# Kernel optimization log

Measured on AMD Instinct MI355X. Metric: run time of the kernel, lower is better.

The kernel has to match this reference:

```python
import jax, jax.numpy as jnp
import numpy as np

EPS = 1e-5
THRESHOLD = 0.2987


def conv3x3(x, w, stride=1):
    # x: [N,C,H,W], w: [O,I,3,3]
    return jax.lax.conv_general_dilated(
        x, w, window_strides=(stride, stride), padding=((1, 1), (1, 1)),
        dimension_numbers=("NCHW", "OIHW", "NCHW"))


def batchnorm_train(x, gamma, beta):
    # training-mode BN: batch statistics over (N,H,W), biased variance
    mean = jnp.mean(x, axis=(0, 2, 3), keepdims=True)
    var = jnp.var(x, axis=(0, 2, 3), keepdims=True)
    xhat = (x - mean) * jax.lax.rsqrt(var + EPS)
    return xhat * gamma[None, :, None, None] + beta[None, :, None, None]


def setup_inputs() -> dict:
    key = jax.random.key(0)
    k = jax.random.split(key, 7)
    N, C, H, W = 64, 128, 64, 64
    x = jax.random.normal(k[0], (N, C, H, W), dtype=jnp.float32)
    w1 = jax.random.normal(k[1], (C, C, 3, 3), dtype=jnp.float32) * (1.0 / np.sqrt(C * 9))
    gamma1 = jnp.ones((C,), dtype=jnp.float32)
    beta1 = jnp.zeros((C,), dtype=jnp.float32)
    w2 = jax.random.normal(k[2], (C, C, 3, 3), dtype=jnp.float32) * (1.0 / np.sqrt(C * 9))
    gamma2 = jnp.ones((C,), dtype=jnp.float32)
    beta2 = jnp.zeros((C,), dtype=jnp.float32)
    return {"x": x, "w1": w1, "gamma1": gamma1, "beta1": beta1,
            "w2": w2, "gamma2": gamma2, "beta2": beta2}


def reference(x, w1, gamma1, beta1, w2, gamma2, beta2):
    shortcut = x  # stride=1, no down_sample
    out = conv3x3(x, w1, stride=1)
    out = batchnorm_train(out, gamma1, beta1)
    out = jax.nn.relu(out)
    # per-(batch,channel) mean over H,W; zero channels whose mean < threshold
    channel_means = jnp.mean(out, axis=(2, 3))               # [N, C]
    mask = (channel_means >= THRESHOLD).astype(out.dtype)     # [N, C]
    out = out * mask[:, :, None, None]
    out = conv3x3(out, w2, stride=1)
    out = batchnorm_train(out, gamma2, beta2)
    out = out + shortcut
    out = jax.nn.relu(out)
    return out
```

## Files before the change

kernel.cpp:

```cpp
#include <hip/hip_runtime.h>

typedef short short8 __attribute__((ext_vector_type(8)));
typedef short short4v __attribute__((ext_vector_type(4)));
typedef float f32x4 __attribute__((ext_vector_type(4)));
typedef unsigned int u32;

#define EPSF 1e-5f
#define THRF 0.2987f

constexpr int N_ = 64, C_ = 128;
constexpr int PLANE = 4096;
constexpr size_t TENSOR = (size_t)N_ * C_ * PLANE;
constexpr int NHW = N_ * PLANE;
constexpr int PUNITS = 66 * 66 * 8;

__device__ __forceinline__ unsigned short f2bf(float f) {
    unsigned u = __float_as_uint(f);
    u += 0x7fffu + ((u >> 16) & 1u);
    return (unsigned short)(u >> 16);
}
__device__ __forceinline__ float bf2f(unsigned short h) {
    return __uint_as_float((unsigned)h << 16);
}
__device__ __forceinline__ void gld16(const unsigned short* g, unsigned short* l) {
    __builtin_amdgcn_global_load_lds(
        (const __attribute__((address_space(1))) u32*)g,
        (__attribute__((address_space(3))) u32*)l, 16, 0, 0);
}

__global__ __launch_bounds__(256) void prep_w_k(const float* __restrict__ w1,
                                                const float* __restrict__ w2,
                                                unsigned short* __restrict__ Wt1,
                                                unsigned short* __restrict__ Wt2) {
    int idx = blockIdx.x * 256 + threadIdx.x;
    const int sel = idx >= 147456;
    const float* src = sel ? w2 : w1;
    unsigned short* dst = sel ? Wt2 : Wt1;
    const int r = idx - sel * 147456;
    const int tap = r >> 14;
    const int rem = r & 16383;
    const int co = rem >> 7, ci = rem & 127;
    const int half = ci >> 6, csh = (ci >> 5) & 1;
    const int s = half * 18 + tap * 2 + csh;
    dst[(size_t)s * 4096 + co * 32 + (ci & 31)] = f2bf(src[(co * 128 + ci) * 9 + tap]);
}

__global__ __launch_bounds__(256) void zero_border_k(unsigned short* __restrict__ io) {
    int idx = blockIdx.x * 256 + threadIdx.x;
    if (idx >= 266240) return;
    const int plane = idx / 2080;
    const int t = idx - plane * 2080;
    int sp;
    if (t < 528) sp = t >> 3;
    else if (t < 1056) sp = 65 * 66 + ((t - 528) >> 3);
    else if (t < 1568) sp = (((t - 1056) >> 3) + 1) * 66;
    else sp = (((t - 1568) >> 3) + 1) * 66 + 65;
    const size_t off = ((size_t)plane * PUNITS + sp * 8 + (t & 7)) * 8;
    *(short8*)&io[off] = (short8){0, 0, 0, 0, 0, 0, 0, 0};
}

__global__ __launch_bounds__(256) void to_nhwc_k(const float* __restrict__ src,
                                                 unsigned short* __restrict__ dst) {
    __shared__ __align__(16) unsigned short tl[64 * 40];
    const int b = blockIdx.x;
    const int c0 = (b & 3) * 32;
    const int h  = (b >> 2) & 63;
    const int n  = b >> 8;
    const int t  = threadIdx.x;
    for (int i = t; i < 512; i += 256) {
        const int cl = i >> 4;
        const int c  = c0 + cl;
        const int w4 = (i & 15) * 4;
        float4 v = *(const float4*)&src[(size_t)(n * 128 + c) * 4096 + h * 64 + w4];
        tl[(w4 + 0) * 40 + cl] = f2bf(v.x);
        tl[(w4 + 1) * 40 + cl] = f2bf(v.y);
        tl[(w4 + 2) * 40 + cl] = f2bf(v.z);
        tl[(w4 + 3) * 40 + cl] = f2bf(v.w);
    }
    __syncthreads();
    const int w = t >> 2, cs = t & 3;
    short8 v = *(const short8*)&tl[w * 40 + cs * 8];
    const int c = c0 + cs * 8;
    const int half = c >> 6, cig = (c >> 3) & 7;
    const int colp = w + 1, rowp = h + 1;
    const size_t off = ((size_t)(half * 64 + n) * PUNITS
                        + (size_t)(rowp * 66 + colp) * 8 + (cig ^ (colp & 7))) * 8;
    *(short8*)&dst[off] = v;
}

template <int STAGE>
__global__ __launch_bounds__(256, 3) void conv_mfma_k(
    const unsigned short* __restrict__ inT, const unsigned short* __restrict__ Wt,
    const float* __restrict__ msA, const float* __restrict__ mhA,
    unsigned short* __restrict__ outB, float* __restrict__ part) {
    __shared__ __align__(16) unsigned short sIn[2112 * 8];
    __shared__ float fS[256], fQ[256];

    const int b  = (blockIdx.x & 7) * 256 + (blockIdx.x >> 3);
    const int h0 = (b & 31) * 2;
    const int n  = b >> 5;
    const int tid  = threadIdx.x;
    const int lane = tid & 63;
    const int wid  = tid >> 6;
    const int co_base = (wid >> 1) * 64;
    const int px_base = (wid & 1) * 64;
    const int lr = lane & 15;
    const int lg = lane >> 4;

    f32x4 acc[4][4];
#pragma unroll
    for (int i = 0; i < 4; ++i)
#pragma unroll
        for (int j = 0; j < 4; ++j) acc[i][j] = (f32x4){0.f, 0.f, 0.f, 0.f};

    const int nc = n * 128;
    const unsigned short* wlane = Wt + (size_t)(co_base + lr) * 32 + lg * 8;

    int ldsQ[4][2][3];
#pragma unroll
    for (int j = 0; j < 4; ++j) {
        const int px = px_base + j * 16 + lr;
        const int r = px >> 6, c = px & 63;
#pragma unroll
        for (int csh = 0; csh < 2; ++csh)
#pragma unroll
            for (int dc = 0; dc < 3; ++dc) {
                const int cig = csh * 4 + lg;
                ldsQ[j][csh][dc] = (r * 66 + c + dc) * 128 + (cig ^ ((c + dc) & 7)) * 16;
            }
    }

    auto stage_in = [&](int half) {
        const unsigned short* src =
            inT + ((size_t)(half * 64 + n) * PUNITS + (size_t)h0 * 66 * 8) * 8;
        if (STAGE == 1) {
            for (int c = wid; c < 33; c += 4)
                gld16(src + (c * 64 + lane) * 8, &sIn[c * 512]);
        } else {
            const int ncb = nc + half * 64;
            for (int i = tid; i < 2112; i += 256) {
                const int sp = i >> 3, ul = i & 7;
                const int rq = sp / 66;
                const int colp = sp - rq * 66;
                const int rp = h0 + rq;
                short8 v = {0, 0, 0, 0, 0, 0, 0, 0};
                if (rp != 0 && rp != 65 && colp != 0 && colp != 65) {
                    v = *(const short8*)&src[i * 8];
                    const int cig = ul ^ (colp & 7);
                    const int cb = ncb + cig * 8;
                    const float4 m0 = *(const float4*)&msA[cb];
                    const float4 m1 = *(const float4*)&msA[cb + 4];
                    const float4 a0 = *(const float4*)&mhA[cb];
                    const float4 a1 = *(const float4*)&mhA[cb + 4];
                    short8 w;
                    w[0] = (short)f2bf(fmaxf(fmaf(bf2f((unsigned short)v[0]), m0.x, a0.x), 0.f));
                    w[1] = (short)f2bf(fmaxf(fmaf(bf2f((unsigned short)v[1]), m0.y, a0.y), 0.f));
                    w[2] = (short)f2bf(fmaxf(fmaf(bf2f((unsigned short)v[2]), m0.z, a0.z), 0.f));
                    w[3] = (short)f2bf(fmaxf(fmaf(bf2f((unsigned short)v[3]), m0.w, a0.w), 0.f));
                    w[4] = (short)f2bf(fmaxf(fmaf(bf2f((unsigned short)v[4]), m1.x, a1.x), 0.f));
                    w[5] = (short)f2bf(fmaxf(fmaf(bf2f((unsigned short)v[5]), m1.y, a1.y), 0.f));
                    w[6] = (short)f2bf(fmaxf(fmaf(bf2f((unsigned short)v[6]), m1.z, a1.z), 0.f));
                    w[7] = (short)f2bf(fmaxf(fmaf(bf2f((unsigned short)v[7]), m1.w, a1.w), 0.f));
                    v = w;
                }
                *(short8*)&sIn[i * 8] = v;
            }
        }
    };

    auto ldw2 = [&](short8* dst, const unsigned short* p) {
#pragma unroll
        for (int i = 0; i < 4; ++i)
            dst[i] = *(const short8*)&p[i * 512];
    };
    auto ldb = [&](short8* bfv, int dr, int dc, int csh) {
#pragma unroll
        for (int j = 0; j < 4; ++j)
            bfv[j] = *(const short8*)((const char*)sIn + ldsQ[j][csh][dc] + dr * 8448);
    };
    auto mm = [&](short8* af, short8* bfv) {
        __builtin_amdgcn_s_setprio(1);
#pragma unroll
        for (int i = 0; i < 4; ++i)
#pragma unroll
            for (int j = 0; j < 4; ++j)
                acc[i][j] = __builtin_amdgcn_mfma_f32_16x16x32_bf16(af[i], bfv[j],
                                                                    acc[i][j], 0, 0, 0);
        __builtin_amdgcn_s_setprio(0);
    };

    short8 afA[4], afB[4], bfv[4];
    const unsigned short* wpA = wlane;
    const unsigned short* wpB = wlane + 4096;

    stage_in(0);
    ldw2(afA, wpA);
    ldw2(afB, wpB);
    __syncthreads();

#pragma unroll
    for (int half = 0; half < 2; ++half) {
#pragma unroll
        for (int it = 0; it < 9; ++it) {
            const int dr = it / 3, dc = it - dr * 3;
            ldb(bfv, dr, dc, 0);
            mm(afA, bfv);
            if (it < 8) { wpA += 8192; ldw2(afA, wpA); }
            ldb(bfv, dr, dc, 1);
            mm(afB, bfv);
            if (it < 8) { wpB += 8192; ldw2(afB, wpB); }
        }
        if (half == 0) {
            wpA += 8192; ldw2(afA, wpA);
            wpB += 8192; ldw2(afB, wpB);
            __syncthreads();
            stage_in(1);
            __syncthreads();
        }
    }

#pragma unroll
    for (int i = 0; i < 4; ++i)
#pragma unroll
        for (int q = 0; q < 4; ++q) {
            float v = acc[i][0][q] + acc[i][1][q] + acc[i][2][q] + acc[i][3][q];
            float w = acc[i][0][q] * acc[i][0][q] + acc[i][1][q] * acc[i][1][q]
                    + acc[i][2][q] * acc[i][2][q] + acc[i][3][q] * acc[i][3][q];
#pragma unroll
            for (int m = 1; m < 16; m <<= 1) {
                v += __shfl_xor(v, m);
                w += __shfl_xor(w, m);
            }
            if (lr == 0) {
                const int colocal = i * 16 + lg * 4 + q;
                fS[wid * 64 + colocal] = v;
                fQ[wid * 64 + colocal] = w;
            }
        }
    __syncthreads();
    if (tid < 128) {
        const int grp = tid >> 6, cl = tid & 63;
        part[(size_t)b * 256 + tid]       = fS[(grp * 2) * 64 + cl] + fS[(grp * 2 + 1) * 64 + cl];
        part[(size_t)b * 256 + 128 + tid] = fQ[(grp * 2) * 64 + cl] + fQ[(grp * 2 + 1) * 64 + cl];
    }

    if (STAGE == 1) {
        const int h = h0 + (px_base >> 6);
        const int rowp = h + 1;
        const size_t plane = (size_t)((co_base >> 6) * 64 + n) * PUNITS * 8;
        const int pg = lg >> 1;
#pragma unroll
        for (int j = 0; j < 4; ++j) {
            const int w = j * 16 + lr;
            const int colp = w + 1;
            const size_t spoff = plane + (size_t)(rowp * 66 + colp) * 8 * 8;
#pragma unroll
            for (int i = 0; i < 4; ++i) {
                u32 p0 = ((u32)f2bf(acc[i][j][1]) << 16) | f2bf(acc[i][j][0]);
                u32 p1 = ((u32)f2bf(acc[i][j][3]) << 16) | f2bf(acc[i][j][2]);
                const u32 q0 = __shfl_xor(p0, 16);
                const u32 q1 = __shfl_xor(p1, 16);
                if ((lg & 1) == 0) {
                    const int cig = (i * 2 + pg) & 7;
                    u32 st4[4] = {p0, p1, q0, q1};
                    *(short8*)&outB[spoff + (size_t)(cig ^ (colp & 7)) * 8] =
                        *(const short8*)st4;
                }
            }
        }
    } else {
        const size_t outN = (size_t)n * 128 * 4096;
#pragma unroll
        for (int i = 0; i < 4; ++i) {
            const int cob = co_base + i * 16 + lg * 4;
#pragma unroll
            for (int q = 0; q < 4; ++q) {
                unsigned short* op = outB + outN + (size_t)(cob + q) * 4096
                                     + h0 * 64 + px_base + lr;
#pragma unroll
                for (int j = 0; j < 4; ++j) op[j * 16] = f2bf(acc[i][j][q]);
            }
        }
    }
}

__global__ __launch_bounds__(256) void bn_finalize_k(const float* __restrict__ part,
                                                     const float* __restrict__ gamma,
                                                     const float* __restrict__ beta,
                                                     float* __restrict__ st) {
    const int c = blockIdx.x;
    float s = 0.f, q = 0.f;
    for (int b = threadIdx.x; b < 2048; b += 256) {
        s += part[(size_t)b * 256 + c];
        q += part[(size_t)b * 256 + 128 + c];
    }
    __shared__ float rs[256], rq[256];
    rs[threadIdx.x] = s; rq[threadIdx.x] = q;
    __syncthreads();
    for (int o = 128; o > 0; o >>= 1) {
        if (threadIdx.x < o) {
            rs[threadIdx.x] += rs[threadIdx.x + o];
            rq[threadIdx.x] += rq[threadIdx.x + o];
        }
        __syncthreads();
    }
    if (threadIdx.x == 0) {
        const float inv  = 1.f / (float)NHW;
        const float mean = rs[0] * inv;
        const float var  = rq[0] * inv - mean * mean;
        const float sc   = gamma[c] * rsqrtf(var + EPSF);
        st[c]       = sc;
        st[C_ + c]  = fmaf(-mean, sc, beta[c]);
    }
}

__global__ __launch_bounds__(256) void maskpart_k(const unsigned short* __restrict__ y1,
                                                  const float* __restrict__ st,
                                                  float* __restrict__ qsum) {
    const int n = blockIdx.x >> 1, half = blockIdx.x & 1;
    const int t = threadIdx.x;
    const int colg = t & 63;
    const int p = t >> 6;
    const int colp = 1 + colg;
    float scv[2][8], shv[2][8], a[2][8];
#pragma unroll
    for (int k = 0; k < 2; ++k)
#pragma unroll
        for (int e = 0; e < 8; ++e) {
            const int c = half * 64 + (2 * p + k) * 8 + e;
            scv[k][e] = st[c];
            shv[k][e] = st[128 + c];
            a[k][e] = 0.f;
        }
    const size_t plane = (size_t)(half * 64 + n) * PUNITS * 8;
    for (int rowp = 1; rowp <= 64; ++rowp) {
        const int sp = rowp * 66 + colp;
#pragma unroll
        for (int k = 0; k < 2; ++k) {
            const int cig = 2 * p + k;
            short8 v = *(const short8*)&y1[plane + ((size_t)sp * 8 + (cig ^ (colp & 7))) * 8];
#pragma unroll
            for (int e = 0; e < 8; ++e)
                a[k][e] += fmaxf(fmaf(bf2f((unsigned short)v[e]), scv[k][e], shv[k][e]), 0.f);
        }
    }
    __shared__ float lds[256][16];
#pragma unroll
    for (int k = 0; k < 2; ++k)
#pragma unroll
        for (int e = 0; e < 8; ++e) lds[t][k * 8 + e] = a[k][e];
    __syncthreads();
    if (t < 64) {
        const int cig = t >> 3, e = t & 7, p2 = cig >> 1, k2 = cig & 1;
        float s = 0.f;
        for (int cg = 0; cg < 64; ++cg) s += lds[p2 * 64 + cg][k2 * 8 + e];
        qsum[(size_t)(n * 2 + half) * 64 + t] = s;
    }
}

__global__ void maskfin_k(const float* __restrict__ qsum, const float* __restrict__ st,
                          float* __restrict__ msA, float* __restrict__ mhA) {
    const int n = blockIdx.x, c = threadIdx.x;
    if (c >= 128) return;
    const int half = c >> 6, cl = c & 63;
    const float s = qsum[(size_t)(n * 2 + half) * 64 + cl];
    const float m = (s * (1.f / 4096.f) >= THRF) ? 1.f : 0.f;
    msA[n * 128 + c] = st[c] * m;
    mhA[n * 128 + c] = st[128 + c] * m;
}

__global__ __launch_bounds__(256) void final_k(const unsigned short* __restrict__ y3,
                                               const float* __restrict__ x,
                                               const float* __restrict__ st,
                                               float* __restrict__ out) {
    const size_t total8 = TENSOR / 8;
    for (size_t g = (size_t)blockIdx.x * 256 + threadIdx.x; g < total8;
         g += (size_t)gridDim.x * 256) {
        const int c = (int)((g >> 9) & (C_ - 1));
        const float sc = st[c], sh = st[C_ + c];
        short8 yv = *(const short8*)&y3[g * 8];
        float4 a0 = ((const float4*)x)[g * 2];
        float4 a1 = ((const float4*)x)[g * 2 + 1];
        float4 o0, o1;
        o0.x = fmaxf(fmaf(bf2f((unsigned short)yv[0]), sc, sh) + a0.x, 0.f);
        o0.y = fmaxf(fmaf(bf2f((unsigned short)yv[1]), sc, sh) + a0.y, 0.f);
        o0.z = fmaxf(fmaf(bf2f((unsigned short)yv[2]), sc, sh) + a0.z, 0.f);
        o0.w = fmaxf(fmaf(bf2f((unsigned short)yv[3]), sc, sh) + a0.w, 0.f);
        o1.x = fmaxf(fmaf(bf2f((unsigned short)yv[4]), sc, sh) + a1.x, 0.f);
        o1.y = fmaxf(fmaf(bf2f((unsigned short)yv[5]), sc, sh) + a1.y, 0.f);
        o1.z = fmaxf(fmaf(bf2f((unsigned short)yv[6]), sc, sh) + a1.z, 0.f);
        o1.w = fmaxf(fmaf(bf2f((unsigned short)yv[7]), sc, sh) + a1.w, 0.f);
        ((float4*)out)[g * 2]     = o0;
        ((float4*)out)[g * 2 + 1] = o1;
    }
}

extern "C" void kernel_launch(void* const* d_in, const int* in_sizes, int n_in,
                              void* d_out, int out_size, void* d_ws, size_t ws_size,
                              hipStream_t stream) {
    const float* x  = (const float*)d_in[0];
    const float* w1 = (const float*)d_in[1];
    const float* g1 = (const float*)d_in[2];
    const float* b1 = (const float*)d_in[3];
    const float* w2 = (const float*)d_in[4];
    const float* g2 = (const float*)d_in[5];
    const float* b2 = (const float*)d_in[6];
    float* out = (float*)d_out;

    unsigned short* y1 = (unsigned short*)d_out;

    char* wsb = (char*)d_ws;
    unsigned short* io  = (unsigned short*)wsb;
    unsigned short* y3b = (unsigned short*)wsb;
    unsigned short* Wt1 = (unsigned short*)(wsb + (size_t)71368704);
    unsigned short* Wt2 = Wt1 + 147456;
    float* part  = (float*)(wsb + (size_t)71368704 + 589824);
    float* st1   = part + 2048 * 256;
    float* st2   = st1 + 256;
    float* qsum  = st2 + 256;
    float* msA   = qsum + 128 * 64;
    float* mhA   = msA + 64 * 128;

    prep_w_k<<<1152, 256, 0, stream>>>(w1, w2, Wt1, Wt2);
    zero_border_k<<<1040, 256, 0, stream>>>(io);
    to_nhwc_k<<<16384, 256, 0, stream>>>(x, io);
    conv_mfma_k<1><<<2048, 256, 0, stream>>>(io, Wt1, nullptr, nullptr, y1, part);
    bn_finalize_k<<<128, 256, 0, stream>>>(part, g1, b1, st1);
    maskpart_k<<<128, 256, 0, stream>>>(y1, st1, qsum);
    maskfin_k<<<64, 128, 0, stream>>>(qsum, st1, msA, mhA);
    conv_mfma_k<2><<<2048, 256, 0, stream>>>(y1, Wt2, msA, mhA, y3b, part);
    bn_finalize_k<<<128, 256, 0, stream>>>(part, g2, b2, st2);
    final_k<<<8192, 256, 0, stream>>>(y3b, x, st2, out);
}
```

Measured before the change: 329.9 us.

## Fuse NCHW-to-bf16 conversion and border padding into first conv staging; merge mask kernels

The first conv now reads fp32 NCHW input directly, converts it to bf16, and writes the swizzled padded tile into LDS with zero halo. This replaces the separate zero_border and to_nhwc passes and the padded intermediate buffer. The mask finalize step is folded into maskpart_k, which removes another launch. The trade-off is that conv1 staging now does strided scalar fp32 loads (8 channels per plane stride) instead of async 16-byte global-to-LDS loads, and each halo row is re-read and re-converted by neighbouring blocks.

```diff
diff --git a/kernel.cpp b/kernel.cpp
--- a/kernel.cpp
+++ b/kernel.cpp
@@ -21,11 +21,6 @@
 }
 __device__ __forceinline__ float bf2f(unsigned short h) {
     return __uint_as_float((unsigned)h << 16);
-}
-__device__ __forceinline__ void gld16(const unsigned short* g, unsigned short* l) {
-    __builtin_amdgcn_global_load_lds(
-        (const __attribute__((address_space(1))) u32*)g,
-        (__attribute__((address_space(3))) u32*)l, 16, 0, 0);
 }
 
 __global__ __launch_bounds__(256) void prep_w_k(const float* __restrict__ w1,
@@ -45,52 +40,10 @@
     dst[(size_t)s * 4096 + co * 32 + (ci & 31)] = f2bf(src[(co * 128 + ci) * 9 + tap]);
 }
 
-__global__ __launch_bounds__(256) void zero_border_k(unsigned short* __restrict__ io) {
-    int idx = blockIdx.x * 256 + threadIdx.x;
-    if (idx >= 266240) return;
-    const int plane = idx / 2080;
-    const int t = idx - plane * 2080;
-    int sp;
-    if (t < 528) sp = t >> 3;
-    else if (t < 1056) sp = 65 * 66 + ((t - 528) >> 3);
-    else if (t < 1568) sp = (((t - 1056) >> 3) + 1) * 66;
-    else sp = (((t - 1568) >> 3) + 1) * 66 + 65;
-    const size_t off = ((size_t)plane * PUNITS + sp * 8 + (t & 7)) * 8;
-    *(short8*)&io[off] = (short8){0, 0, 0, 0, 0, 0, 0, 0};
-}
-
-__global__ __launch_bounds__(256) void to_nhwc_k(const float* __restrict__ src,
-                                                 unsigned short* __restrict__ dst) {
-    __shared__ __align__(16) unsigned short tl[64 * 40];
-    const int b = blockIdx.x;
-    const int c0 = (b & 3) * 32;
-    const int h  = (b >> 2) & 63;
-    const int n  = b >> 8;
-    const int t  = threadIdx.x;
-    for (int i = t; i < 512; i += 256) {
-        const int cl = i >> 4;
-        const int c  = c0 + cl;
-        const int w4 = (i & 15) * 4;
-        float4 v = *(const float4*)&src[(size_t)(n * 128 + c) * 4096 + h * 64 + w4];
-        tl[(w4 + 0) * 40 + cl] = f2bf(v.x);
-        tl[(w4 + 1) * 40 + cl] = f2bf(v.y);
-        tl[(w4 + 2) * 40 + cl] = f2bf(v.z);
-        tl[(w4 + 3) * 40 + cl] = f2bf(v.w);
-    }
-    __syncthreads();
-    const int w = t >> 2, cs = t & 3;
-    short8 v = *(const short8*)&tl[w * 40 + cs * 8];
-    const int c = c0 + cs * 8;
-    const int half = c >> 6, cig = (c >> 3) & 7;
-    const int colp = w + 1, rowp = h + 1;
-    const size_t off = ((size_t)(half * 64 + n) * PUNITS
-                        + (size_t)(rowp * 66 + colp) * 8 + (cig ^ (colp & 7))) * 8;
-    *(short8*)&dst[off] = v;
-}
-
 template <int STAGE>
 __global__ __launch_bounds__(256, 3) void conv_mfma_k(
-    const unsigned short* __restrict__ inT, const unsigned short* __restrict__ Wt,
+    const unsigned short* __restrict__ inT, const float* __restrict__ xin,
+    const unsigned short* __restrict__ Wt,
     const float* __restrict__ msA, const float* __restrict__ mhA,
     unsigned short* __restrict__ outB, float* __restrict__ part) {
     __shared__ __align__(16) unsigned short sIn[2112 * 8];
@@ -131,12 +84,30 @@
     }
 
     auto stage_in = [&](int half) {
-        const unsigned short* src =
-            inT + ((size_t)(half * 64 + n) * PUNITS + (size_t)h0 * 66 * 8) * 8;
         if (STAGE == 1) {
-            for (int c = wid; c < 33; c += 4)
-                gld16(src + (c * 64 + lane) * 8, &sIn[c * 512]);
+            const float* xs = xin + (size_t)(nc + half * 64) * PLANE;
+#pragma unroll
+            for (int base = 0; base < 2112; base += 256) {
+                const int idx = base + tid;
+                if (idx < 2112) {
+                    const int cig  = idx / 264;
+                    const int sp   = idx - cig * 264;
+                    const int rq   = sp / 66;
+                    const int colp = sp - rq * 66;
+                    const int gh = h0 + rq - 1;
+                    const int gw = colp - 1;
+                    short8 v = {0, 0, 0, 0, 0, 0, 0, 0};
+                    if ((unsigned)gh < 64u && (unsigned)gw < 64u) {
+                        const float* p = xs + (size_t)cig * 8 * PLANE + gh * 64 + gw;
+#pragma unroll
+                        for (int e = 0; e < 8; ++e) v[e] = (short)f2bf(p[(size_t)e * PLANE]);
+                    }
+                    *(short8*)&sIn[(sp * 8 + (cig ^ (colp & 7))) * 8] = v;
+                }
+            }
         } else {
+            const unsigned short* src =
+                inT + ((size_t)(half * 64 + n) * PUNITS + (size_t)h0 * 66 * 8) * 8;
             const int ncb = nc + half * 64;
             for (int i = tid; i < 2112; i += 256) {
                 const int sp = i >> 3, ul = i & 7;
@@ -316,7 +287,8 @@
 
 __global__ __launch_bounds__(256) void maskpart_k(const unsigned short* __restrict__ y1,
                                                   const float* __restrict__ st,
-                                                  float* __restrict__ qsum) {
+                                                  float* __restrict__ msA,
+                                                  float* __restrict__ mhA) {
     const int n = blockIdx.x >> 1, half = blockIdx.x & 1;
     const int t = threadIdx.x;
     const int colg = t & 63;
@@ -354,19 +326,11 @@
         const int cig = t >> 3, e = t & 7, p2 = cig >> 1, k2 = cig & 1;
         float s = 0.f;
         for (int cg = 0; cg < 64; ++cg) s += lds[p2 * 64 + cg][k2 * 8 + e];
-        qsum[(size_t)(n * 2 + half) * 64 + t] = s;
-    }
-}
-
-__global__ void maskfin_k(const float* __restrict__ qsum, const float* __restrict__ st,
-                          float* __restrict__ msA, float* __restrict__ mhA) {
-    const int n = blockIdx.x, c = threadIdx.x;
-    if (c >= 128) return;
-    const int half = c >> 6, cl = c & 63;
-    const float s = qsum[(size_t)(n * 2 + half) * 64 + cl];
-    const float m = (s * (1.f / 4096.f) >= THRF) ? 1.f : 0.f;
-    msA[n * 128 + c] = st[c] * m;
-    mhA[n * 128 + c] = st[128 + c] * m;
+        const int c = half * 64 + t;
+        const float m = (s * (1.f / 4096.f) >= THRF) ? 1.f : 0.f;
+        msA[n * 128 + c] = st[c] * m;
+        mhA[n * 128 + c] = st[128 + c] * m;
+    }
 }
 
 __global__ __launch_bounds__(256) void final_k(const unsigned short* __restrict__ y3,
@@ -410,25 +374,20 @@
     unsigned short* y1 = (unsigned short*)d_out;
 
     char* wsb = (char*)d_ws;
-    unsigned short* io  = (unsigned short*)wsb;
     unsigned short* y3b = (unsigned short*)wsb;
-    unsigned short* Wt1 = (unsigned short*)(wsb + (size_t)71368704);
+    unsigned short* Wt1 = (unsigned short*)(wsb + (size_t)67108864);
     unsigned short* Wt2 = Wt1 + 147456;
-    float* part  = (float*)(wsb + (size_t)71368704 + 589824);
-    float* st1   = part + 2048 * 256;
-    float* st2   = st1 + 256;
-    float* qsum  = st2 + 256;
-    float* msA   = qsum + 128 * 64;
-    float* mhA   = msA + 64 * 128;
+    float* part = (float*)(wsb + (size_t)67108864 + 589824);
+    float* st1  = part + 2048 * 256;
+    float* st2  = st1 + 256;
+    float* msA  = st2 + 256;
+    float* mhA  = msA + 64 * 128;
 
     prep_w_k<<<1152, 256, 0, stream>>>(w1, w2, Wt1, Wt2);
-    zero_border_k<<<1040, 256, 0, stream>>>(io);
-    to_nhwc_k<<<16384, 256, 0, stream>>>(x, io);
-    conv_mfma_k<1><<<2048, 256, 0, stream>>>(io, Wt1, nullptr, nullptr, y1, part);
+    conv_mfma_k<1><<<2048, 256, 0, stream>>>(nullptr, x, Wt1, nullptr, nullptr, y1, part);
     bn_finalize_k<<<128, 256, 0, stream>>>(part, g1, b1, st1);
-    maskpart_k<<<128, 256, 0, stream>>>(y1, st1, qsum);
-    maskfin_k<<<64, 128, 0, stream>>>(qsum, st1, msA, mhA);
-    conv_mfma_k<2><<<2048, 256, 0, stream>>>(y1, Wt2, msA, mhA, y3b, part);
+    maskpart_k<<<128, 256, 0, stream>>>(y1, st1, msA, mhA);
+    conv_mfma_k<2><<<2048, 256, 0, stream>>>(y1, nullptr, Wt2, msA, mhA, y3b, part);
     bn_finalize_k<<<128, 256, 0, stream>>>(part, g2, b2, st2);
     final_k<<<8192, 256, 0, stream>>>(y3b, x, st2, out);
 }
```

After: 331.4 us. About the same (+0.5%).
